# Optimization experiments

Hardware: AMD Instinct MI355X
Metric: run time of the kernel (lower is better)

## Reference

```python
import jax, jax.numpy as jnp
import numpy as np

N_NODES = 50000
N_EDGES = 800000
N_GRAPHS = 512
D = 128
NUM_GIN_LAYERS = 4
BN_EPS = 1e-5


def setup_inputs() -> dict:
    key = jax.random.key(0)
    ks = jax.random.split(key, 10)
    h = jax.random.normal(ks[0], (N_NODES, D), dtype=jnp.float32)
    src = jax.random.randint(ks[1], (N_EDGES,), 0, N_NODES, dtype=jnp.int32)
    dst = jax.random.randint(ks[2], (N_EDGES,), 0, N_NODES, dtype=jnp.int32)
    graph_id = jnp.sort(jax.random.randint(ks[3], (N_NODES,), 0, N_GRAPHS, dtype=jnp.int32))
    scale = 1.0 / np.sqrt(D)
    W1s = jax.random.normal(ks[4], (NUM_GIN_LAYERS, D, D), dtype=jnp.float32) * scale
    W2s = jax.random.normal(ks[5], (NUM_GIN_LAYERS, D, D), dtype=jnp.float32) * scale
    bn1_g = jnp.ones((NUM_GIN_LAYERS, D), jnp.float32)
    bn1_b = jnp.zeros((NUM_GIN_LAYERS, D), jnp.float32)
    bn2_g = jnp.ones((NUM_GIN_LAYERS, D), jnp.float32)
    bn2_b = jnp.zeros((NUM_GIN_LAYERS, D), jnp.float32)
    pred_W = jax.random.normal(ks[6], (NUM_GIN_LAYERS + 1, D, D), dtype=jnp.float32) * scale
    pred_b = jnp.zeros((NUM_GIN_LAYERS + 1, D), jnp.float32)
    return {"h": h, "src": src, "dst": dst, "graph_id": graph_id,
            "W1s": W1s, "W2s": W2s, "bn1_g": bn1_g, "bn1_b": bn1_b,
            "bn2_g": bn2_g, "bn2_b": bn2_b, "pred_W": pred_W, "pred_b": pred_b}


def _batch_norm(x, gamma, beta):
    # training-mode BN over the node axis
    mean = jnp.mean(x, axis=0)
    var = jnp.var(x, axis=0)
    return (x - mean) * jax.lax.rsqrt(var + BN_EPS) * gamma + beta


def reference(h, src, dst, graph_id, W1s, W2s, bn1_g, bn1_b, bn2_g, bn2_b, pred_W, pred_b):
    n = h.shape[0]
    hidden_rep = [h]
    for i in range(NUM_GIN_LAYERS):
        # GINConv, eps=0: (1+eps)*h + sum over in-neighbors (scatter-sum over edges)
        agg = jax.ops.segment_sum(h[src], dst, num_segments=n)
        z = h + agg
        # two-layer MLP: Linear(no bias) -> BN -> ReLU -> Linear(no bias)
        z = jax.nn.relu(_batch_norm(z @ W1s[i], bn1_g[i], bn1_b[i]))
        z = z @ W2s[i]
        # outer BN + ReLU
        h = jax.nn.relu(_batch_norm(z, bn2_g[i], bn2_b[i]))
        hidden_rep.append(h)
    # graph readout: per-graph max pool over each layer's representation,
    # then per-layer linear prediction summed (dropout is identity in eval)
    score = jnp.zeros((N_GRAPHS, pred_W.shape[-1]), h.dtype)
    for i, hr in enumerate(hidden_rep):
        pooled = jax.ops.segment_max(hr, graph_id, num_segments=N_GRAPHS,
                                     indices_are_sorted=True)
        score = score + pooled @ pred_W[i] + pred_b[i]
    return score
```

## Files before the change

### kernel.cpp

```cpp
#include <hip/hip_runtime.h>

#define N_NODES 50000
#define N_EDGES 800000
#define N_GRAPHS 512
#define DIM 128
#define NLAYERS 4
#define BN_EPS 1e-5f
#define NTILE (N_NODES / 16)
#define POIS ((int)0xAAAAAAAA)
#define NREP 8

#define NBUCK 80
#define CAPB 12288
#define EPB 1600
#define NBIN 500

typedef unsigned short u16;
typedef float f32x2 __attribute__((ext_vector_type(2)));
typedef float f32x4 __attribute__((ext_vector_type(4)));
typedef short bf16x8 __attribute__((ext_vector_type(8)));

__device__ __forceinline__ short f2bs(float f) {
    union { float f; unsigned u; } v; v.f = f;
    unsigned r = v.u + 0x7FFFu + ((v.u >> 16) & 1u);
    return (short)(r >> 16);
}
__device__ __forceinline__ float bu2f(unsigned u) {
    union { unsigned u; float f; } v; v.u = u << 16;
    return v.f;
}
__device__ __forceinline__ unsigned packbf(float x, float y) {
    return ((unsigned)(u16)f2bs(y) << 16) | (unsigned)(u16)f2bs(x);
}

__device__ __forceinline__ void foldbn(const float* __restrict__ st,
                                       const float* __restrict__ gamma,
                                       const float* __restrict__ beta,
                                       float* absm, int tid) {
    if (tid < 128) {
        float s = 0.f, sq = 0.f;
#pragma unroll
        for (int j = 0; j < NREP; j++) {
            s += st[j * 256 + tid];
            sq += st[j * 256 + 128 + tid];
        }
        float mean = s * (1.f / N_NODES);
        float var = sq * (1.f / N_NODES) - mean * mean;
        float a = gamma[tid] * rsqrtf(var + BN_EPS);
        absm[tid] = a;
        absm[DIM + tid] = beta[tid] - mean * a;
    }
}

__global__ __launch_bounds__(256) void k_prepbin(const float* __restrict__ h,
                                                 const float* __restrict__ W1s,
                                                 const float* __restrict__ W2s,
                                                 const int* __restrict__ gid,
                                                 const int* __restrict__ src,
                                                 const int* __restrict__ dst,
                                                 unsigned* __restrict__ hb,
                                                 short* __restrict__ wt,
                                                 int* __restrict__ gs, int* __restrict__ ge,
                                                 unsigned* __restrict__ eb,
                                                 int* __restrict__ gcur) {
    __shared__ int hist[NBUCK], base[NBUCK], lcur[NBUCK];
    int bid = blockIdx.x, tid = threadIdx.x;
    if (bid >= 6250) {
        int bbid = bid - 6250;
        if (tid < NBUCK) hist[tid] = 0;
        __syncthreads();
        int e0 = bbid * EPB;
        unsigned rec[7]; int rb[7];
#pragma unroll
        for (int k = 0; k < 7; k++) {
            int idx = tid + k * 256;
            rb[k] = -1;
            if (idx < EPB) {
                int s = src[e0 + idx], d = dst[e0 + idx];
                rec[k] = ((unsigned)d << 16) | (unsigned)s;
                int x = d / 6250;
                int sub = (d - x * 6250) / 625;
                rb[k] = x + 8 * sub;
                atomicAdd(&hist[rb[k]], 1);
            }
        }
        __syncthreads();
        if (tid < NBUCK) {
            int old = atomicAdd(&gcur[tid], hist[tid]);
            base[tid] = old - POIS;
            lcur[tid] = 0;
        }
        __syncthreads();
#pragma unroll
        for (int k = 0; k < 7; k++) {
            if (rb[k] >= 0) {
                int p = atomicAdd(&lcur[rb[k]], 1);
                eb[rb[k] * CAPB + base[rb[k]] + p] = rec[k];
            }
        }
        return;
    }
    int gtid = bid * 256 + tid;
    {
        f32x4 v = *(const f32x4*)(h + gtid * 4);
        uint2 pp;
        pp.x = packbf(v.x, v.y);
        pp.y = packbf(v.z, v.w);
        *(uint2*)(hb + gtid * 2) = pp;
    }
    if (gtid < 8 * 16384) {
        int m = gtid >> 14, r = gtid & 16383, n = r >> 7, k = r & 127;
        const float* W = (m < 4) ? (W1s + m * 16384) : (W2s + (m - 4) * 16384);
        wt[gtid] = f2bs(W[k * DIM + n]);
    }
    if (gtid < N_NODES) {
        int g = gid[gtid];
        if (gtid == 0 || gid[gtid - 1] != g) gs[g] = gtid;
        if (gtid == N_NODES - 1 || gid[gtid + 1] != g) ge[g] = gtid + 1;
    }
}

__global__ __launch_bounds__(256) void k_fillpool0(const unsigned* __restrict__ eb,
                                                   const int* __restrict__ gcur,
                                                   int* __restrict__ begA,
                                                   int* __restrict__ endA,
                                                   u16* __restrict__ eix,
                                                   const float* __restrict__ h,
                                                   const int* __restrict__ gs,
                                                   const int* __restrict__ ge,
                                                   float* __restrict__ pool4) {
    __shared__ int hist[625], begL[625], sm[256];
    __shared__ f32x2 psm[256];
    int bid = blockIdx.x, tid = threadIdx.x;
    if (bid < NBUCK) {
        int x = bid & 7, sub = bid >> 3;
        int n0 = x * 6250 + sub * 625;
        int mybase = 0, mycnt = 0;
        for (int r = 0; r < NBUCK; r++) {
            int c = gcur[r] - POIS;
            int rx = r & 7, rs = r >> 3;
            if (rx < x || (rx == x && rs < sub)) mybase += c;
            if (r == bid) mycnt = c;
        }
        for (int i = tid; i < 625; i += 256) hist[i] = 0;
        __syncthreads();
        const unsigned* my = eb + bid * CAPB;
        for (int i = tid; i < mycnt; i += 256) {
            int dl = (int)(my[i] >> 16) - n0;
            atomicAdd(&hist[dl], 1);
        }
        __syncthreads();
        int carry = 0;
        for (int c = 0; c < 3; c++) {
            int idx = c * 256 + tid;
            int v = (idx < 625) ? hist[idx] : 0;
            int xv = v;
            sm[tid] = xv; __syncthreads();
#pragma unroll
            for (int d = 1; d < 256; d <<= 1) {
                int y = (tid >= d) ? sm[tid - d] : 0;
                __syncthreads();
                sm[tid] = xv = xv + y;
                __syncthreads();
            }
            if (idx < 625) begL[idx] = mybase + carry + xv - v;
            int ct = sm[255];
            __syncthreads();
            carry += ct;
        }
        __syncthreads();
        for (int i = tid; i < 625; i += 256) {
            int b = begL[i];
            begA[n0 + i] = b;
            endA[n0 + i] = b + hist[i];
        }
        __syncthreads();
        for (int i = tid; i < mycnt; i += 256) {
            unsigned rc = my[i];
            int dl = (int)(rc >> 16) - n0;
            int p = atomicAdd(&begL[dl], 1);
            eix[p] = (u16)(rc & 0xFFFFu);
        }
        return;
    }
    int pb = bid - NBUCK;
    int g = pb >> 2, sub = pb & 3;
    int c2 = (tid & 63) * 2, ro = tid >> 6;
    int beg = gs[g], end = ge[g];
    f32x2 mx = (f32x2){-3.402823e38f, -3.402823e38f};
    if (beg >= 0 && end <= N_NODES) {
        for (int r = beg + sub * 4 + ro; r < end; r += 16) {
            f32x2 v = *(const f32x2*)(h + r * DIM + c2);
            mx.x = fmaxf(mx.x, v.x);
            mx.y = fmaxf(mx.y, v.y);
        }
    }
    psm[tid] = mx;
    __syncthreads();
    if (ro == 0) {
        f32x2 mA0 = psm[tid], mA1 = psm[tid + 64];
        f32x2 mB0 = psm[tid + 128], mB1 = psm[tid + 192];
        f32x2 a, b;
        a.x = fmaxf(mA0.x, mA1.x); a.y = fmaxf(mA0.y, mA1.y);
        b.x = fmaxf(mB0.x, mB1.x); b.y = fmaxf(mB0.y, mB1.y);
        *(f32x2*)(pool4 + (pb * 2) * DIM + c2) = a;
        *(f32x2*)(pool4 + (pb * 2 + 1) * DIM + c2) = b;
    }
}

__global__ __launch_bounds__(128) void k_gather0(const unsigned* __restrict__ hp,
                                                 const int* __restrict__ begA,
                                                 const int* __restrict__ endA,
                                                 const u16* __restrict__ eix,
                                                 unsigned* __restrict__ Za) {
    int node = blockIdx.x * 2 + (threadIdx.x >> 6);
    int lane = threadIdx.x & 63;
    float ax = 0.f, ay = 0.f;
#define TX(w, rx, ry)                                         \
    {                                                         \
        rx += bu2f((w) & 0xffffu); ry += bu2f((w) >> 16);     \
    }
    TX(hp[node * 64 + lane], ax, ay);
    int beg = begA[node];
    int end = endA[node];
    int e = beg;
    if ((e & 1) && e < end) {
        unsigned ww = hp[eix[e] * 64 + lane];
        TX(ww, ax, ay);
        e++;
    }
    const unsigned* ep = (const unsigned*)eix;
    for (; e + 8 <= end; e += 8) {
        int k = e >> 1;
        unsigned p0 = ep[k], p1 = ep[k + 1], p2 = ep[k + 2], p3 = ep[k + 3];
        unsigned w0 = hp[(p0 & 0xffffu) * 64 + lane], w1 = hp[(p0 >> 16) * 64 + lane];
        unsigned w2 = hp[(p1 & 0xffffu) * 64 + lane], w3 = hp[(p1 >> 16) * 64 + lane];
        unsigned w4 = hp[(p2 & 0xffffu) * 64 + lane], w5 = hp[(p2 >> 16) * 64 + lane];
        unsigned w6 = hp[(p3 & 0xffffu) * 64 + lane], w7 = hp[(p3 >> 16) * 64 + lane];
        TX(w0, ax, ay); TX(w1, ax, ay); TX(w2, ax, ay); TX(w3, ax, ay);
        TX(w4, ax, ay); TX(w5, ax, ay); TX(w6, ax, ay); TX(w7, ax, ay);
    }
    for (; e + 2 <= end; e += 2) {
        unsigned pp = ep[e >> 1];
        unsigned w0 = hp[(pp & 0xffffu) * 64 + lane], w1 = hp[(pp >> 16) * 64 + lane];
        TX(w0, ax, ay); TX(w1, ax, ay);
    }
    if (e < end) {
        unsigned ww = hp[eix[e] * 64 + lane];
        TX(ww, ax, ay);
    }
#undef TX
    Za[node * 64 + lane] = packbf(ax, ay);
}

__global__ __launch_bounds__(128) void k_poolgather(const unsigned* __restrict__ Zr,
                                                    const float* __restrict__ stats,
                                                    const float* __restrict__ gamma,
                                                    const float* __restrict__ beta,
                                                    const int* __restrict__ gs,
                                                    const int* __restrict__ ge,
                                                    float* __restrict__ pool4,
                                                    const int* __restrict__ begA,
                                                    const int* __restrict__ endA,
                                                    const u16* __restrict__ eix,
                                                    unsigned* __restrict__ Za) {
    __shared__ float absm[256];
    __shared__ f32x2 psm[128];
    int bid = blockIdx.x, tid = threadIdx.x;
    foldbn(stats, gamma, beta, absm, tid);
    __syncthreads();
    if (bid < 4096) {
        int g = bid >> 3, sub = bid & 7;
        int ci = tid & 63, ro = tid >> 6;
        int beg = gs[g], end = ge[g];
        f32x2 a = *(const f32x2*)(absm + ci * 2);
        f32x2 b = *(const f32x2*)(absm + DIM + ci * 2);
        f32x2 mx = (f32x2){-3.402823e38f, -3.402823e38f};
        if (beg >= 0 && end <= N_NODES) {
            for (int r = beg + sub * 2 + ro; r < end; r += 16) {
                unsigned w = Zr[r * 64 + ci];
                float vx = fmaxf(a.x * bu2f(w & 0xffffu) + b.x, 0.f);
                float vy = fmaxf(a.y * bu2f(w >> 16) + b.y, 0.f);
                mx.x = fmaxf(mx.x, vx);
                mx.y = fmaxf(mx.y, vy);
            }
        }
        psm[tid] = mx;
        __syncthreads();
        if (ro == 0) {
            f32x2 m0 = psm[tid], m1 = psm[tid + 64];
            m0.x = fmaxf(m0.x, m1.x);
            m0.y = fmaxf(m0.y, m1.y);
            *(f32x2*)(pool4 + bid * DIM + ci * 2) = m0;
        }
        return;
    }
    int node = (bid - 4096) * 2 + (tid >> 6);
    int lane = tid & 63;
    float a0 = absm[2 * lane], a1 = absm[2 * lane + 1];
    float b0 = absm[DIM + 2 * lane], b1 = absm[DIM + 2 * lane + 1];
#define TX(w, rx, ry)                                         \
    {                                                         \
        float _x = bu2f((w) & 0xffffu), _y = bu2f((w) >> 16); \
        _x = fmaxf(a0 * _x + b0, 0.f);                        \
        _y = fmaxf(a1 * _y + b1, 0.f);                        \
        rx += _x; ry += _y;                                   \
    }
    float ax = 0.f, ay = 0.f;
    TX(Zr[node * 64 + lane], ax, ay);
    int beg = begA[node];
    int end = endA[node];
    int e = beg;
    if ((e & 1) && e < end) {
        unsigned ww = Zr[eix[e] * 64 + lane];
        TX(ww, ax, ay);
        e++;
    }
    const unsigned* ep = (const unsigned*)eix;
    for (; e + 8 <= end; e += 8) {
        int k = e >> 1;
        unsigned p0 = ep[k], p1 = ep[k + 1], p2 = ep[k + 2], p3 = ep[k + 3];
        unsigned w0 = Zr[(p0 & 0xffffu) * 64 + lane], w1 = Zr[(p0 >> 16) * 64 + lane];
        unsigned w2 = Zr[(p1 & 0xffffu) * 64 + lane], w3 = Zr[(p1 >> 16) * 64 + lane];
        unsigned w4 = Zr[(p2 & 0xffffu) * 64 + lane], w5 = Zr[(p2 >> 16) * 64 + lane];
        unsigned w6 = Zr[(p3 & 0xffffu) * 64 + lane], w7 = Zr[(p3 >> 16) * 64 + lane];
        TX(w0, ax, ay); TX(w1, ax, ay); TX(w2, ax, ay); TX(w3, ax, ay);
        TX(w4, ax, ay); TX(w5, ax, ay); TX(w6, ax, ay); TX(w7, ax, ay);
    }
    for (; e + 2 <= end; e += 2) {
        unsigned pp = ep[e >> 1];
        unsigned w0 = Zr[(pp & 0xffffu) * 64 + lane], w1 = Zr[(pp >> 16) * 64 + lane];
        TX(w0, ax, ay); TX(w1, ax, ay);
    }
    if (e < end) {
        unsigned ww = Zr[eix[e] * 64 + lane];
        TX(ww, ax, ay);
    }
#undef TX
    Za[node * 64 + lane] = packbf(ax, ay);
}

template <bool XF>
__global__ __launch_bounds__(256, 3) void k_gemm(const unsigned* __restrict__ X,
                                                 const short* __restrict__ wt,
                                                 const float* __restrict__ statsPrev,
                                                 const float* __restrict__ gamma,
                                                 const float* __restrict__ beta,
                                                 unsigned* __restrict__ OUT,
                                                 float* __restrict__ statsDst) {
    __shared__ short wls[128][136];
    __shared__ float tbuf[4][16][68];
    __shared__ float absm[256];
    __shared__ float smst[256];
    const int tid = threadIdx.x, bid = blockIdx.x;
    const int lane = tid & 63, wid = tid >> 6;
    const int ln15 = lane & 15, q = lane >> 4;
    float (*buf)[68] = tbuf[wid];

    {
        int r = tid >> 1, hh = tid & 1;
        const uint4* s4 = (const uint4*)(wt + r * 128 + hh * 64);
        uint4* d4 = (uint4*)&wls[r][hh * 64];
#pragma unroll
        for (int i = 0; i < 8; i++) d4[i] = s4[i];
    }
    if (XF) foldbn(statsPrev, gamma, beta, absm, tid);
    smst[tid] = 0.f;
    __syncthreads();

    float sac[8], qac[8];
#pragma unroll
    for (int t = 0; t < 8; t++) { sac[t] = 0.f; qac[t] = 0.f; }

    int tile = bid * 4 + wid;
    if (tile < NTILE) {
        f32x4 aA[4], aB[4], bA[4], bB[4];
        if (XF) {
#pragma unroll
            for (int s = 0; s < 4; s++) {
                int k0 = s * 32 + q * 8;
                aA[s] = *(const f32x4*)(absm + k0);
                aB[s] = *(const f32x4*)(absm + k0 + 4);
                bA[s] = *(const f32x4*)(absm + DIM + k0);
                bB[s] = *(const f32x4*)(absm + DIM + k0 + 4);
            }
        }
        const unsigned* xr = X + (tile * 16 + ln15) * 64;
        bf16x8 afr[4];
        if constexpr (!XF) {
#pragma unroll
            for (int s = 0; s < 4; s++)
                afr[s] = *(const bf16x8*)(xr + s * 16 + q * 4);
        } else {
#pragma unroll
            for (int s = 0; s < 4; s++) {
                uint4 w4v = *(const uint4*)(xr + s * 16 + q * 4);
                float v0 = fmaxf(aA[s].x * bu2f(w4v.x & 0xffffu) + bA[s].x, 0.f);
                float v1 = fmaxf(aA[s].y * bu2f(w4v.x >> 16) + bA[s].y, 0.f);
                float v2 = fmaxf(aA[s].z * bu2f(w4v.y & 0xffffu) + bA[s].z, 0.f);
                float v3 = fmaxf(aA[s].w * bu2f(w4v.y >> 16) + bA[s].w, 0.f);
                float v4 = fmaxf(aB[s].x * bu2f(w4v.z & 0xffffu) + bB[s].x, 0.f);
                float v5 = fmaxf(aB[s].y * bu2f(w4v.z >> 16) + bB[s].y, 0.f);
                float v6 = fmaxf(aB[s].z * bu2f(w4v.w & 0xffffu) + bB[s].z, 0.f);
                float v7 = fmaxf(aB[s].w * bu2f(w4v.w >> 16) + bB[s].w, 0.f);
                bf16x8 a;
                a[0] = f2bs(v0); a[1] = f2bs(v1); a[2] = f2bs(v2); a[3] = f2bs(v3);
                a[4] = f2bs(v4); a[5] = f2bs(v5); a[6] = f2bs(v6); a[7] = f2bs(v7);
                afr[s] = a;
            }
        }
        f32x4 acc[8];
#pragma unroll
        for (int t = 0; t < 8; t++) acc[t] = (f32x4){0.f, 0.f, 0.f, 0.f};
#pragma unroll
        for (int s = 0; s < 4; s++) {
#pragma unroll
            for (int t = 0; t < 8; t++) {
                bf16x8 bfr = *(const bf16x8*)&wls[t * 16 + ln15][s * 32 + q * 8];
                acc[t] = __builtin_amdgcn_mfma_f32_16x16x32_bf16(afr[s], bfr, acc[t], 0, 0, 0);
            }
        }
#pragma unroll
        for (int t = 0; t < 8; t++) {
            float s_l = 0.f, q_l = 0.f;
#pragma unroll
            for (int r = 0; r < 4; r++) {
                float v = acc[t][r];
                s_l += v;
                q_l += v * v;
            }
            s_l += __shfl_xor(s_l, 16); s_l += __shfl_xor(s_l, 32);
            q_l += __shfl_xor(q_l, 16); q_l += __shfl_xor(q_l, 32);
            sac[t] = s_l;
            qac[t] = q_l;
        }
#pragma unroll
        for (int ch = 0; ch < 2; ch++) {
#pragma unroll
            for (int t2 = 0; t2 < 4; t2++) {
                int t = ch * 4 + t2;
#pragma unroll
                for (int r = 0; r < 4; r++)
                    buf[q * 4 + r][t2 * 16 + ln15] = acc[t][r];
            }
#pragma unroll
            for (int rr = 0; rr < 4; rr++) {
                int lr = rr * 4 + q;
                f32x4 v = *(const f32x4*)&buf[lr][ln15 * 4];
                uint2 pp;
                pp.x = packbf(v.x, v.y);
                pp.y = packbf(v.z, v.w);
                *(uint2*)(OUT + (tile * 16 + lr) * 64 + ch * 32 + ln15 * 2) = pp;
            }
        }
    }
    if (lane < 16) {
#pragma unroll
        for (int t = 0; t < 8; t++) {
            atomicAdd(&smst[t * 16 + ln15], sac[t]);
            atomicAdd(&smst[128 + t * 16 + ln15], qac[t]);
        }
    }
    __syncthreads();
    atomicAdd(statsDst + (bid & (NREP - 1)) * 256 + tid, smst[tid]);
}

__global__ __launch_bounds__(256) void k_pool(const unsigned* __restrict__ Zr,
                                              const float* __restrict__ stats,
                                              const float* __restrict__ gamma,
                                              const float* __restrict__ beta,
                                              const int* __restrict__ gs,
                                              const int* __restrict__ ge,
                                              float* __restrict__ pool4) {
    __shared__ float absm[256];
    __shared__ f32x2 psm[256];
    int bid = blockIdx.x, tid = threadIdx.x;
    int g = bid >> 2, sub = bid & 3;
    foldbn(stats, gamma, beta, absm, tid);
    __syncthreads();
    int ci = tid & 63, ro = tid >> 6;
    int beg = gs[g], end = ge[g];
    f32x2 a = *(const f32x2*)(absm + ci * 2);
    f32x2 b = *(const f32x2*)(absm + DIM + ci * 2);
    f32x2 mx = (f32x2){-3.402823e38f, -3.402823e38f};
    if (beg >= 0 && end <= N_NODES) {
        for (int r = beg + sub * 4 + ro; r < end; r += 16) {
            unsigned w = Zr[r * 64 + ci];
            float vx = fmaxf(a.x * bu2f(w & 0xffffu) + b.x, 0.f);
            float vy = fmaxf(a.y * bu2f(w >> 16) + b.y, 0.f);
            mx.x = fmaxf(mx.x, vx);
            mx.y = fmaxf(mx.y, vy);
        }
    }
    psm[tid] = mx;
    __syncthreads();
    if (ro == 0) {
        f32x2 mA0 = psm[tid], mA1 = psm[tid + 64];
        f32x2 mB0 = psm[tid + 128], mB1 = psm[tid + 192];
        f32x2 aa, bb;
        aa.x = fmaxf(mA0.x, mA1.x); aa.y = fmaxf(mA0.y, mA1.y);
        bb.x = fmaxf(mB0.x, mB1.x); bb.y = fmaxf(mB0.y, mB1.y);
        *(f32x2*)(pool4 + (bid * 2) * DIM + ci * 2) = aa;
        *(f32x2*)(pool4 + (bid * 2 + 1) * DIM + ci * 2) = bb;
    }
}

__global__ __launch_bounds__(640) void k_readout(const float* __restrict__ pool4,
                                                 const float* __restrict__ predW,
                                                 const float* __restrict__ predb,
                                                 float* __restrict__ out) {
    __shared__ float pl[5][DIM];
    __shared__ float ps[5][DIM];
    int g = blockIdx.x, t = threadIdx.x;
    int l = t >> 7, c = t & 127;
    {
        const float* p = pool4 + l * (N_GRAPHS * 8 * DIM) + g * 8 * DIM + c;
        float m = p[0];
#pragma unroll
        for (int j = 1; j < 8; j++) m = fmaxf(m, p[j * DIM]);
        pl[l][c] = m;
    }
    __syncthreads();
    float acc = 0.f;
    const float* W = predW + l * DIM * DIM;
    const float* prow = pl[l];
#pragma unroll 8
    for (int k = 0; k < DIM; k++) acc += prow[k] * W[k * DIM + c];
    ps[l][c] = acc;
    __syncthreads();
    if (t < DIM) {
        float s = 0.f;
#pragma unroll
        for (int ll = 0; ll < 5; ll++) s += ps[ll][c] + predb[ll * DIM + c];
        out[g * DIM + c] = s;
    }
}

extern "C" void kernel_launch(void* const* d_in, const int* in_sizes, int n_in,
                              void* d_out, int out_size, void* d_ws, size_t ws_size,
                              hipStream_t stream) {
    const float* h_in = (const float*)d_in[0];
    const int* src = (const int*)d_in[1];
    const int* dst = (const int*)d_in[2];
    const int* gid = (const int*)d_in[3];
    const float* W1s = (const float*)d_in[4];
    const float* W2s = (const float*)d_in[5];
    const float* bn1g = (const float*)d_in[6];
    const float* bn1b = (const float*)d_in[7];
    const float* bn2g = (const float*)d_in[8];
    const float* bn2b = (const float*)d_in[9];
    const float* predW = (const float*)d_in[10];
    const float* predb = (const float*)d_in[11];

    char* ws = (char*)d_ws;
    unsigned* hb = (unsigned*)(ws);
    unsigned* Za = (unsigned*)(ws + 12800000);
    unsigned* Yb = (unsigned*)(ws + 25600000);
    unsigned* Zr = (unsigned*)(ws + 38400000);
    short* wt = (short*)(ws + 51200000);
    float* pool4 = (float*)(ws + 51527680);
    int* begA = (int*)(ws + 62013440);
    int* endA = (int*)(ws + 62213440);
    u16* eix = (u16*)(ws + 62413440);
    int* gs = (int*)(ws + 64013440);
    int* ge = (int*)(ws + 64015488);
    float* stats = (float*)(ws + 64017536);
    unsigned* eb = (unsigned*)(ws + 25600000);
    int* gcur = (int*)(ws + 25600000 + 8388608);
    float* out = (float*)d_out;

    const int PSTRIDE = N_GRAPHS * 8 * DIM;

    k_prepbin<<<6750, 256, 0, stream>>>(h_in, W1s, W2s, gid, src, dst, hb, wt, gs, ge, eb, gcur);
    k_fillpool0<<<NBUCK + 2048, 256, 0, stream>>>(eb, gcur, begA, endA, eix, h_in, gs, ge, pool4);

    k_gather0<<<25000, 128, 0, stream>>>(hb, begA, endA, eix, Za);
    k_gemm<false><<<782, 256, 0, stream>>>(Za, wt + 0 * 16384, nullptr, nullptr, nullptr,
                                           Yb, stats + 0 * (NREP * 256));
    k_gemm<true><<<782, 256, 0, stream>>>(Yb, wt + 4 * 16384, stats + 0 * (NREP * 256),
                                          bn1g, bn1b, Zr, stats + 1 * (NREP * 256));
    for (int l = 1; l < NLAYERS; l++) {
        k_poolgather<<<29096, 128, 0, stream>>>(Zr, stats + ((l - 1) * 2 + 1) * (NREP * 256),
                                                bn2g + (l - 1) * DIM, bn2b + (l - 1) * DIM,
                                                gs, ge, pool4 + l * PSTRIDE,
                                                begA, endA, eix, Za);
        k_gemm<false><<<782, 256, 0, stream>>>(Za, wt + l * 16384, nullptr, nullptr, nullptr,
                                               Yb, stats + (l * 2) * (NREP * 256));
        k_gemm<true><<<782, 256, 0, stream>>>(Yb, wt + (4 + l) * 16384,
                                              stats + (l * 2) * (NREP * 256), bn1g + l * DIM,
                                              bn1b + l * DIM, Zr,
                                              stats + (l * 2 + 1) * (NREP * 256));
    }
    k_pool<<<2048, 256, 0, stream>>>(Zr, stats + 7 * (NREP * 256), bn2g + 3 * DIM,
                                     bn2b + 3 * DIM, gs, ge, pool4 + 4 * PSTRIDE);
    k_readout<<<512, 640, 0, stream>>>(pool4, predW, predb, out);
}
```

Before: 440.4 us.

## Fuse final-layer pooling into readout, hoist GEMM input loads, pool layer0 from bf16

Removes the separate k_pool launch by computing the last layer's BN+ReLU+segment max directly inside k_readout, with 5 row-groups per graph block. Layer-0 pooling in k_fillpool0 now reads the bf16 copy of h instead of fp32, which halves the bytes read. The GEMM kernels issue their activation row loads before staging the weights into LDS so the global load latency overlaps. Risks: the fused readout does the last-layer pool with 512 blocks and scalar per-column loads, and layer-0 pooling now rounds inputs to bf16, so the max is no longer exact.

```diff
diff --git a/kernel.cpp b/kernel.cpp
--- a/kernel.cpp
+++ b/kernel.cpp
@@ -125,7 +125,7 @@
                                                    int* __restrict__ begA,
                                                    int* __restrict__ endA,
                                                    u16* __restrict__ eix,
-                                                   const float* __restrict__ h,
+                                                   const unsigned* __restrict__ hb,
                                                    const int* __restrict__ gs,
                                                    const int* __restrict__ ge,
                                                    float* __restrict__ pool4) {
@@ -185,14 +185,14 @@
     }
     int pb = bid - NBUCK;
     int g = pb >> 2, sub = pb & 3;
-    int c2 = (tid & 63) * 2, ro = tid >> 6;
+    int ci = tid & 63, ro = tid >> 6;
     int beg = gs[g], end = ge[g];
     f32x2 mx = (f32x2){-3.402823e38f, -3.402823e38f};
     if (beg >= 0 && end <= N_NODES) {
         for (int r = beg + sub * 4 + ro; r < end; r += 16) {
-            f32x2 v = *(const f32x2*)(h + r * DIM + c2);
-            mx.x = fmaxf(mx.x, v.x);
-            mx.y = fmaxf(mx.y, v.y);
+            unsigned w = hb[r * 64 + ci];
+            mx.x = fmaxf(mx.x, bu2f(w & 0xffffu));
+            mx.y = fmaxf(mx.y, bu2f(w >> 16));
         }
     }
     psm[tid] = mx;
@@ -203,8 +203,8 @@
         f32x2 a, b;
         a.x = fmaxf(mA0.x, mA1.x); a.y = fmaxf(mA0.y, mA1.y);
         b.x = fmaxf(mB0.x, mB1.x); b.y = fmaxf(mB0.y, mB1.y);
-        *(f32x2*)(pool4 + (pb * 2) * DIM + c2) = a;
-        *(f32x2*)(pool4 + (pb * 2 + 1) * DIM + c2) = b;
+        *(f32x2*)(pool4 + (pb * 2) * DIM + ci * 2) = a;
+        *(f32x2*)(pool4 + (pb * 2 + 1) * DIM + ci * 2) = b;
     }
 }
 
@@ -357,6 +357,13 @@
     const int ln15 = lane & 15, q = lane >> 4;
     float (*buf)[68] = tbuf[wid];
 
+    int tile = bid * 4 + wid;
+    uint4 xv[4];
+    if (tile < NTILE) {
+        const unsigned* xr = X + (tile * 16 + ln15) * 64;
+#pragma unroll
+        for (int s = 0; s < 4; s++) xv[s] = *(const uint4*)(xr + s * 16 + q * 4);
+    }
     {
         int r = tid >> 1, hh = tid & 1;
         const uint4* s4 = (const uint4*)(wt + r * 128 + hh * 64);
@@ -372,10 +379,13 @@
 #pragma unroll
     for (int t = 0; t < 8; t++) { sac[t] = 0.f; qac[t] = 0.f; }
 
-    int tile = bid * 4 + wid;
     if (tile < NTILE) {
-        f32x4 aA[4], aB[4], bA[4], bB[4];
-        if (XF) {
+        bf16x8 afr[4];
+        if constexpr (!XF) {
+#pragma unroll
+            for (int s = 0; s < 4; s++) afr[s] = *(bf16x8*)&xv[s];
+        } else {
+            f32x4 aA[4], aB[4], bA[4], bB[4];
 #pragma unroll
             for (int s = 0; s < 4; s++) {
                 int k0 = s * 32 + q * 8;
@@ -384,17 +394,9 @@
                 bA[s] = *(const f32x4*)(absm + DIM + k0);
                 bB[s] = *(const f32x4*)(absm + DIM + k0 + 4);
             }
-        }
-        const unsigned* xr = X + (tile * 16 + ln15) * 64;
-        bf16x8 afr[4];
-        if constexpr (!XF) {
-#pragma unroll
-            for (int s = 0; s < 4; s++)
-                afr[s] = *(const bf16x8*)(xr + s * 16 + q * 4);
-        } else {
 #pragma unroll
             for (int s = 0; s < 4; s++) {
-                uint4 w4v = *(const uint4*)(xr + s * 16 + q * 4);
+                uint4 w4v = xv[s];
                 float v0 = fmaxf(aA[s].x * bu2f(w4v.x & 0xffffu) + bA[s].x, 0.f);
                 float v1 = fmaxf(aA[s].y * bu2f(w4v.x >> 16) + bA[s].y, 0.f);
                 float v2 = fmaxf(aA[s].z * bu2f(w4v.y & 0xffffu) + bA[s].z, 0.f);
@@ -465,55 +467,54 @@
     atomicAdd(statsDst + (bid & (NREP - 1)) * 256 + tid, smst[tid]);
 }
 
-__global__ __launch_bounds__(256) void k_pool(const unsigned* __restrict__ Zr,
-                                              const float* __restrict__ stats,
-                                              const float* __restrict__ gamma,
-                                              const float* __restrict__ beta,
-                                              const int* __restrict__ gs,
-                                              const int* __restrict__ ge,
-                                              float* __restrict__ pool4) {
-    __shared__ float absm[256];
-    __shared__ f32x2 psm[256];
-    int bid = blockIdx.x, tid = threadIdx.x;
-    int g = bid >> 2, sub = bid & 3;
-    foldbn(stats, gamma, beta, absm, tid);
-    __syncthreads();
-    int ci = tid & 63, ro = tid >> 6;
-    int beg = gs[g], end = ge[g];
-    f32x2 a = *(const f32x2*)(absm + ci * 2);
-    f32x2 b = *(const f32x2*)(absm + DIM + ci * 2);
-    f32x2 mx = (f32x2){-3.402823e38f, -3.402823e38f};
-    if (beg >= 0 && end <= N_NODES) {
-        for (int r = beg + sub * 4 + ro; r < end; r += 16) {
-            unsigned w = Zr[r * 64 + ci];
-            float vx = fmaxf(a.x * bu2f(w & 0xffffu) + b.x, 0.f);
-            float vy = fmaxf(a.y * bu2f(w >> 16) + b.y, 0.f);
-            mx.x = fmaxf(mx.x, vx);
-            mx.y = fmaxf(mx.y, vy);
-        }
-    }
-    psm[tid] = mx;
-    __syncthreads();
-    if (ro == 0) {
-        f32x2 mA0 = psm[tid], mA1 = psm[tid + 64];
-        f32x2 mB0 = psm[tid + 128], mB1 = psm[tid + 192];
-        f32x2 aa, bb;
-        aa.x = fmaxf(mA0.x, mA1.x); aa.y = fmaxf(mA0.y, mA1.y);
-        bb.x = fmaxf(mB0.x, mB1.x); bb.y = fmaxf(mB0.y, mB1.y);
-        *(f32x2*)(pool4 + (bid * 2) * DIM + ci * 2) = aa;
-        *(f32x2*)(pool4 + (bid * 2 + 1) * DIM + ci * 2) = bb;
-    }
-}
-
 __global__ __launch_bounds__(640) void k_readout(const float* __restrict__ pool4,
+                                                 const unsigned* __restrict__ Zr,
+                                                 const float* __restrict__ stats,
+                                                 const float* __restrict__ gamma,
+                                                 const float* __restrict__ beta,
+                                                 const int* __restrict__ gs,
+                                                 const int* __restrict__ ge,
                                                  const float* __restrict__ predW,
                                                  const float* __restrict__ predb,
                                                  float* __restrict__ out) {
     __shared__ float pl[5][DIM];
     __shared__ float ps[5][DIM];
+    __shared__ float absm[256];
     int g = blockIdx.x, t = threadIdx.x;
     int l = t >> 7, c = t & 127;
+    foldbn(stats, gamma, beta, absm, t);
+    __syncthreads();
     {
+        int beg = gs[g], end = ge[g];
+        float a = absm[c], b = absm[DIM + c];
+        float m4 = -3.402823e38f;
+        if (beg >= 0 && end <= N_NODES) {
+            int cd = c >> 1;
+            int r = beg + l;
+            for (; r + 5 < end; r += 10) {
+                unsigned w0 = Zr[r * 64 + cd];
+                unsigned w1 = Zr[(r + 5) * 64 + cd];
+                float v0 = bu2f((c & 1) ? (w0 >> 16) : (w0 & 0xffffu));
+                float v1 = bu2f((c & 1) ? (w1 >> 16) : (w1 & 0xffffu));
+                m4 = fmaxf(m4, fmaxf(a * v0 + b, 0.f));
+                m4 = fmaxf(m4, fmaxf(a * v1 + b, 0.f));
+            }
+            if (r < end) {
+                unsigned w0 = Zr[r * 64 + cd];
+                float v0 = bu2f((c & 1) ? (w0 >> 16) : (w0 & 0xffffu));
+                m4 = fmaxf(m4, fmaxf(a * v0 + b, 0.f));
+            }
+        }
+        ps[l][c] = m4;
+    }
+    __syncthreads();
+    if (t < DIM) {
+        float m = ps[0][t];
+#pragma unroll
+        for (int j = 1; j < 5; j++) m = fmaxf(m, ps[j][t]);
+        pl[4][t] = m;
+    }
+    if (l < 4) {
         const float* p = pool4 + l * (N_GRAPHS * 8 * DIM) + g * 8 * DIM + c;
         float m = p[0];
 #pragma unroll
@@ -572,7 +573,7 @@
     const int PSTRIDE = N_GRAPHS * 8 * DIM;
 
     k_prepbin<<<6750, 256, 0, stream>>>(h_in, W1s, W2s, gid, src, dst, hb, wt, gs, ge, eb, gcur);
-    k_fillpool0<<<NBUCK + 2048, 256, 0, stream>>>(eb, gcur, begA, endA, eix, h_in, gs, ge, pool4);
+    k_fillpool0<<<NBUCK + 2048, 256, 0, stream>>>(eb, gcur, begA, endA, eix, hb, gs, ge, pool4);
 
     k_gather0<<<25000, 128, 0, stream>>>(hb, begA, endA, eix, Za);
     k_gemm<false><<<782, 256, 0, stream>>>(Za, wt + 0 * 16384, nullptr, nullptr, nullptr,
@@ -591,7 +592,7 @@
                                               bn1b + l * DIM, Zr,
                                               stats + (l * 2 + 1) * (NREP * 256));
     }
-    k_pool<<<2048, 256, 0, stream>>>(Zr, stats + 7 * (NREP * 256), bn2g + 3 * DIM,
-                                     bn2b + 3 * DIM, gs, ge, pool4 + 4 * PSTRIDE);
-    k_readout<<<512, 640, 0, stream>>>(pool4, predW, predb, out);
-}
+    k_readout<<<512, 640, 0, stream>>>(pool4, Zr, stats + 7 * (NREP * 256),
+                                       bn2g + 3 * DIM, bn2b + 3 * DIM, gs, ge,
+                                       predW, predb, out);
+}
```

New measurement: 439.0 us. Within noise of the previous version (-0.3%).
